# Kernel tuning notes

Measured on AMD Instinct MI355X. Metric: run time of the kernel, lower is better.

## Reference

```python
import jax, jax.numpy as jnp
import numpy as np

N, E, D_IN, HID, OUT, H = 50000, 800000, 64, 128, 128, 8


def _lin(key, fan_in, fan_out, bias=True):
    k1, k2 = jax.random.split(key)
    W = jax.random.normal(k1, (fan_in, fan_out), jnp.float32) / np.sqrt(fan_in)
    if bias:
        b = jax.random.normal(k2, (fan_out,), jnp.float32) * 0.01
        return W, b
    return (W,)


def setup_inputs() -> dict:
    key = jax.random.key(0)
    ks = jax.random.split(key, 40)
    inp = {
        "x": jax.random.normal(ks[0], (N, D_IN), jnp.float32),
        "edge_index": jax.random.randint(ks[1], (2, E), 0, N, jnp.int64),
        "edge_attr": jax.random.normal(ks[2], (E, D_IN), jnp.float32),
    }
    dims = [(D_IN, HID), (HID, HID), (HID, OUT)]  # (in, heads*out_ch) per layer
    ki = 3
    for l, (di, do) in enumerate(dims):
        inp[f"Wq{l}"], inp[f"bq{l}"] = _lin(ks[ki], di, do); ki += 1
        inp[f"Wk{l}"], inp[f"bk{l}"] = _lin(ks[ki], di, do); ki += 1
        inp[f"Wv{l}"], inp[f"bv{l}"] = _lin(ks[ki], di, do); ki += 1
        (inp[f"We{l}"],) = _lin(ks[ki], D_IN, do, bias=False); ki += 1
        inp[f"Ws{l}"], inp[f"bs{l}"] = _lin(ks[ki], di, do); ki += 1
    for l in range(2):
        inp[f"g{l}"] = jnp.ones((HID,), jnp.float32)
        inp[f"be{l}"] = jnp.zeros((HID,), jnp.float32)
    return inp


def _transformer_conv(x, src, dst, edge_attr, Wq, bq, Wk, bk, Wv, bv, We, Ws, bs):
    n = x.shape[0]
    hc = Wq.shape[1]
    c = hc // H
    q = (x @ Wq + bq).reshape(n, H, c)
    k = (x @ Wk + bk).reshape(n, H, c)
    v = (x @ Wv + bv).reshape(n, H, c)
    e = (edge_attr @ We).reshape(-1, H, c)  # [E,H,c]
    ke = k[src] + e                          # edge-wise key + edge proj
    alpha = jnp.einsum("ehc,ehc->eh", q[dst], ke) / jnp.sqrt(jnp.float32(c))
    m = jax.ops.segment_max(alpha, dst, num_segments=n)
    m = jnp.where(jnp.isfinite(m), m, 0.0)
    p = jnp.exp(alpha - m[dst])
    s = jax.ops.segment_sum(p, dst, num_segments=n)
    a = p / (s[dst] + 1e-16)                 # segment softmax over in-edges
    msg = (v[src] + e) * a[..., None]
    out = jax.ops.segment_sum(msg, dst, num_segments=n).reshape(n, hc)
    return out + x @ Ws + bs                 # root/skip connection


def _bn(x, g, b):
    mu = jnp.mean(x, axis=0)
    var = jnp.mean(jnp.square(x - mu), axis=0)
    return g * (x - mu) * jax.lax.rsqrt(var + 1e-5) + b


def reference(x, edge_index, edge_attr,
              Wq0, bq0, Wk0, bk0, Wv0, bv0, We0, Ws0, bs0,
              Wq1, bq1, Wk1, bk1, Wv1, bv1, We1, Ws1, bs1,
              Wq2, bq2, Wk2, bk2, Wv2, bv2, We2, Ws2, bs2,
              g0, be0, g1, be1):
    src, dst = edge_index[0], edge_index[1]
    h = _transformer_conv(x, src, dst, edge_attr, Wq0, bq0, Wk0, bk0, Wv0, bv0, We0, Ws0, bs0)
    h = jax.nn.relu(_bn(h, g0, be0))
    h = _transformer_conv(h, src, dst, edge_attr, Wq1, bq1, Wk1, bk1, Wv1, bv1, We1, Ws1, bs1)
    h = jax.nn.relu(_bn(h, g1, be1))
    h = _transformer_conv(h, src, dst, edge_attr, Wq2, bq2, Wk2, bk2, Wv2, bv2, We2, Ws2, bs2)
    return h, edge_attr
```

## Files before the change

### kernel.cpp

```cpp
#include <hip/hip_runtime.h>
#include <hip/hip_bf16.h>

typedef __attribute__((ext_vector_type(8))) short short8;
typedef __attribute__((ext_vector_type(4))) float f32x4;
typedef unsigned short ushort_t;
typedef __attribute__((ext_vector_type(2))) unsigned short ushort2v;
typedef __attribute__((ext_vector_type(2))) unsigned int uint2v;
typedef __attribute__((ext_vector_type(4))) unsigned int uint4v;

static __device__ __forceinline__ ushort_t f2bf(float x) {
    __hip_bfloat16 h = __float2bfloat16(x);
    return *(ushort_t*)&h;
}
static __device__ __forceinline__ float bflo(unsigned int u) { return __uint_as_float(u << 16); }
static __device__ __forceinline__ float bfhi(unsigned int u) { return __uint_as_float(u & 0xffff0000u); }
static __device__ __forceinline__ float bfu(ushort_t u) { return __uint_as_float((unsigned int)u << 16); }

template <int CTRL>
static __device__ __forceinline__ float dpp_xadd(float x) {
    int y = __builtin_amdgcn_update_dpp(0, __float_as_int(x), CTRL, 0xF, 0xF, true);
    return x + __int_as_float(y);
}


__global__ void hist_kernel(const int* __restrict__ dst, int E, int* __restrict__ hist) {
    int i = blockIdx.x * blockDim.x + threadIdx.x;
    if (i < E) atomicAdd(&hist[dst[i]], 1);
}

__global__ __launch_bounds__(1024) void scan_block_kernel(
    const int* __restrict__ hist, int n, int* __restrict__ row_ptr, int* __restrict__ bsums)
{
    __shared__ int lds[1024];
    int tid = threadIdx.x;
    int i = blockIdx.x * 1024 + tid;
    int vv = (i < n) ? hist[i] : 0;
    lds[tid] = vv;
    __syncthreads();
    for (int off = 1; off < 1024; off <<= 1) {
        int t = (tid >= off) ? lds[tid - off] : 0;
        __syncthreads();
        lds[tid] += t;
        __syncthreads();
    }
    if (i < n) row_ptr[i] = lds[tid] - vv;
    if (tid == 1023) bsums[blockIdx.x] = lds[1023];
}

__global__ void scan_tops_kernel(int* __restrict__ bsums, int nb) {
    if (threadIdx.x == 0 && blockIdx.x == 0) {
        int run = 0;
        for (int i = 0; i < nb; i++) { int t = bsums[i]; bsums[i] = run; run += t; }
    }
}

__global__ __launch_bounds__(256) void scan_add_kernel(
    const int* __restrict__ bsums, int n, int total,
    int* __restrict__ row_ptr, int* __restrict__ cursor)
{
    int i = blockIdx.x * blockDim.x + threadIdx.x;
    if (i < n) {
        int vv = row_ptr[i] + bsums[i >> 10];
        row_ptr[i] = vv;
        cursor[i] = vv;
    }
    if (i == 0) row_ptr[n] = total;
}

__global__ void scatter_kernel(const int* __restrict__ src, const int* __restrict__ dst, int E,
                               int* __restrict__ cursor, int* __restrict__ inv, int* __restrict__ srcs) {
    int i = blockIdx.x * blockDim.x + threadIdx.x;
    if (i < E) {
        int d = dst[i];
        int pos = atomicAdd(&cursor[d], 1);
        inv[i] = pos;
        srcs[pos] = src[i];
    }
}

__global__ __launch_bounds__(256) void copy_permute_kernel(
    const float* __restrict__ edge_attr, const int* __restrict__ inv, int E,
    float* __restrict__ out_pass, ushort_t* __restrict__ ea)
{
    int idx = blockIdx.x * blockDim.x + threadIdx.x;
    if (idx >= E * 8) return;
    int i = idx >> 3, seg = idx & 7;
    const float* s = edge_attr + (size_t)i * 64 + seg * 8;
    float4 f0 = *(const float4*)s;
    float4 f1 = *(const float4*)(s + 4);
    float* d = out_pass + (size_t)i * 64 + seg * 8;
    *(float4*)d = f0;
    *(float4*)(d + 4) = f1;
    short8 o;
    o[0] = f2bf(f0.x); o[1] = f2bf(f0.y); o[2] = f2bf(f0.z); o[3] = f2bf(f0.w);
    o[4] = f2bf(f1.x); o[5] = f2bf(f1.y); o[6] = f2bf(f1.z); o[7] = f2bf(f1.w);
    int pos = inv[i];
    *(short8*)(ea + (size_t)pos * 64 + seg * 8) = o;
}

struct PackArgs {
    const float* We[3];
    const float* Wn[3][4];
    const float* bb[3][4];
};

__global__ __launch_bounds__(256) void pack_all_kernel(
    PackArgs pa, ushort_t* __restrict__ BpackE, ushort_t* __restrict__ BpackN,
    float* __restrict__ biasc)
{
    int idx = blockIdx.x * blockDim.x + threadIdx.x;
    if (idx < 24576) {
        int j = idx & 7, lane = (idx >> 3) & 63, kk = (idx >> 9) & 1,
            t = (idx >> 10) & 7, layer = idx >> 13;
        int kdim = kk * 32 + (lane >> 4) * 8 + j;
        int ncol = t * 16 + (lane & 15);
        BpackE[idx] = f2bf(pa.We[layer][kdim * 128 + ncol]);
    } else if (idx < 188416) {
        int local = idx - 24576;
        int layer, DI;
        if (local < 32768) { layer = 0; DI = 64; }
        else if (local < 98304) { layer = 1; DI = 128; local -= 32768; }
        else { layer = 2; DI = 128; local -= 98304; }
        int NKF = DI >> 5;
        int j = local & 7, lane = (local >> 3) & 63;
        int rest = local >> 9;
        int kf = rest % NKF, t = rest / NKF;
        int kdim = kf * 32 + (lane >> 4) * 8 + j;
        int ncol = t * 16 + (lane & 15);
        BpackN[layer * 65536 + local] = f2bf(pa.Wn[layer][ncol >> 7][kdim * 128 + (ncol & 127)]);
    } else if (idx < 189952) {
        int local = idx - 188416;
        int layer = local >> 9, i = local & 511;
        biasc[layer * 512 + i] = pa.bb[layer][i >> 7][i & 127];
    }
}

template <int DI, bool BN>
__global__ __launch_bounds__(256) void node_gemm_mfma_kernel(
    const float* __restrict__ hin, int N,
    const ushort_t* __restrict__ Bpack, const float* __restrict__ biasc,
    const float* __restrict__ scale, const float* __restrict__ shift,
    float* __restrict__ qout, unsigned int* __restrict__ kvout,
    float* __restrict__ skipout)
{
    constexpr int NKF = DI / 32;
    __shared__ float ctile[64][132];
    __shared__ ushort_t ctileK[64][136];
    int wave = threadIdx.x >> 6;
    int lane = threadIdx.x & 63;
    int tid = threadIdx.x;
    int base = blockIdx.x * 64;
    int m0 = base + wave * 16;

    int mrow = min(m0 + (lane & 15), N - 1);
    const float* arow = hin + (size_t)mrow * DI;
    int koff = (lane >> 4) * 8;

    short8 a[NKF];
#pragma unroll
    for (int kf = 0; kf < NKF; kf++) {
        float4 fa = *(const float4*)(arow + kf * 32 + koff);
        float4 fb = *(const float4*)(arow + kf * 32 + koff + 4);
        if constexpr (BN) {
            int c0 = kf * 32 + koff;
            float4 sa = *(const float4*)(scale + c0);
            float4 sb = *(const float4*)(scale + c0 + 4);
            float4 ha = *(const float4*)(shift + c0);
            float4 hb = *(const float4*)(shift + c0 + 4);
            fa.x = fmaxf(fa.x * sa.x + ha.x, 0.f);
            fa.y = fmaxf(fa.y * sa.y + ha.y, 0.f);
            fa.z = fmaxf(fa.z * sa.z + ha.z, 0.f);
            fa.w = fmaxf(fa.w * sa.w + ha.w, 0.f);
            fb.x = fmaxf(fb.x * sb.x + hb.x, 0.f);
            fb.y = fmaxf(fb.y * sb.y + hb.y, 0.f);
            fb.z = fmaxf(fb.z * sb.z + hb.z, 0.f);
            fb.w = fmaxf(fb.w * sb.w + hb.w, 0.f);
        }
        short8 t;
        t[0] = f2bf(fa.x); t[1] = f2bf(fa.y); t[2] = f2bf(fa.z); t[3] = f2bf(fa.w);
        t[4] = f2bf(fb.x); t[5] = f2bf(fb.y); t[6] = f2bf(fb.z); t[7] = f2bf(fb.w);
        a[kf] = t;
    }

    const short8* Bp = (const short8*)Bpack;
    f32x4 acc[32];
#pragma unroll
    for (int t = 0; t < 32; t++) acc[t] = (f32x4){0.f, 0.f, 0.f, 0.f};
#pragma unroll
    for (int t = 0; t < 32; t++) {
#pragma unroll
        for (int kf = 0; kf < NKF; kf++)
            acc[t] = __builtin_amdgcn_mfma_f32_16x16x32_bf16(a[kf], Bp[(t * NKF + kf) * 64 + lane], acc[t], 0, 0, 0);
    }

    int crow = (lane >> 4) * 4;
    int ccol = lane & 15;

#pragma unroll
    for (int t8 = 0; t8 < 8; t8++) {
        float bb = biasc[t8 * 16 + ccol];
#pragma unroll
        for (int r = 0; r < 4; r++)
            ctile[wave * 16 + crow + r][t8 * 16 + ccol] = acc[t8][r] + bb;
    }
    __syncthreads();
#pragma unroll
    for (int it = 0; it < 8; it++) {
        int idx4 = it * 256 + tid;
        int row = idx4 >> 5;
        int c4 = idx4 & 31;
        int gr = base + row;
        if (gr < N)
            *(float4*)(qout + (size_t)gr * 128 + c4 * 4) = *(const float4*)&ctile[row][c4 * 4];
    }
    __syncthreads();

#pragma unroll
    for (int t8 = 0; t8 < 8; t8++) {
        float bb = biasc[128 + t8 * 16 + ccol];
#pragma unroll
        for (int r = 0; r < 4; r++)
            ctileK[wave * 16 + crow + r][t8 * 16 + ccol] = f2bf(acc[8 + t8][r] + bb);
    }
#pragma unroll
    for (int t8 = 0; t8 < 8; t8++) {
        float bb = biasc[256 + t8 * 16 + ccol];
#pragma unroll
        for (int r = 0; r < 4; r++)
            ctile[wave * 16 + crow + r][t8 * 16 + ccol] = acc[16 + t8][r] + bb;
    }
    __syncthreads();
#pragma unroll
    for (int it = 0; it < 4; it++) {
        int idx8 = it * 256 + tid;
        int row = idx8 >> 4;
        int c8 = idx8 & 15;
        int gr = base + row;
        if (gr < N) {
            const float* vs = &ctile[row][c8 * 8];
            uint4v o0, o1;
#pragma unroll
            for (int i = 0; i < 4; i++) {
                ushort2v kp2 = *(const ushort2v*)&ctileK[row][c8 * 8 + 2 * i];
                unsigned int kp = (unsigned int)kp2[0] | ((unsigned int)kp2[1] << 16);
                unsigned int vp = (unsigned int)f2bf(vs[2 * i]) | ((unsigned int)f2bf(vs[2 * i + 1]) << 16);
                if (i < 2) { o0[2 * i] = kp; o0[2 * i + 1] = vp; }
                else       { o1[2 * (i - 2)] = kp; o1[2 * (i - 2) + 1] = vp; }
            }
            unsigned int* dp = kvout + (size_t)gr * 128 + c8 * 8;
            *(uint4v*)dp = o0;
            *(uint4v*)(dp + 4) = o1;
        }
    }
    __syncthreads();

#pragma unroll
    for (int t8 = 0; t8 < 8; t8++) {
        float bb = biasc[384 + t8 * 16 + ccol];
#pragma unroll
        for (int r = 0; r < 4; r++)
            ctile[wave * 16 + crow + r][t8 * 16 + ccol] = acc[24 + t8][r] + bb;
    }
    __syncthreads();
#pragma unroll
    for (int it = 0; it < 8; it++) {
        int idx4 = it * 256 + tid;
        int row = idx4 >> 5;
        int c4 = idx4 & 31;
        int gr = base + row;
        if (gr < N)
            *(float4*)(skipout + (size_t)gr * 128 + c4 * 4) = *(const float4*)&ctile[row][c4 * 4];
    }
}

#define PROCESS8(B, MASKED)                                                      \
    {                                                                            \
        ushort2v eev[8];                                                         \
        float p[8];                                                              \
        _Pragma("unroll")                                                        \
        for (int u = 0; u < 8; u++)                                              \
            eev[u] = *(const ushort2v*)&elds[wave][(B) * 8 + u][2 * lane];       \
        _Pragma("unroll")                                                        \
        for (int u = 0; u < 8; u++) {                                            \
            uint2v kvp = kvr[(B) * 8 + u];                                       \
            p[u] = qq.x * (bflo(kvp[0]) + bfu(eev[u][0]))                        \
                 + qq.y * (bfhi(kvp[0]) + bfu(eev[u][1]));                       \
        }                                                                        \
        _Pragma("unroll")                                                        \
        for (int u = 0; u < 8; u++) {                                            \
            p[u] = dpp_xadd<0xB1>(p[u]);                                         \
            p[u] = dpp_xadd<0x4E>(p[u]);                                         \
            p[u] = dpp_xadd<0x141>(p[u]);       \
        }                                                                        \
        _Pragma("unroll")                                                        \
        for (int u = 0; u < 8; u++) {                                            \
            float wv = __expf(p[u]);                                             \
            if ((MASKED) && (c0 + (B) * 8 + u >= je)) wv = 0.f;                  \
            uint2v kvp = kvr[(B) * 8 + u];                                       \
            acc0 += wv * (bflo(kvp[1]) + bfu(eev[u][0]));                        \
            acc1 += wv * (bfhi(kvp[1]) + bfu(eev[u][1]));                        \
            sw += wv;                                                            \
        }                                                                        \
    }

__global__ __launch_bounds__(256) void agg_fused_kernel(
    const int* __restrict__ row_ptr, const int* __restrict__ srcs,
    const float* __restrict__ q, const unsigned int* __restrict__ kvbuf,
    const ushort_t* __restrict__ ea, const ushort_t* __restrict__ BpackWe,
    float* __restrict__ hout, int N)
{
    __shared__ ushort_t elds[4][16][136];
    int tid = threadIdx.x;
    int wave = tid >> 6, lane = tid & 63;
    int n = blockIdx.x * 4 + wave;
    if (n >= N) return;

    const short8* BpG = (const short8*)BpackWe;
    short8 bq[16];
#pragma unroll
    for (int i = 0; i < 16; i++) bq[i] = BpG[i * 64 + lane];

    const float2* q2 = (const float2*)q;
    float2* h2 = (float2*)hout;

    int ch = lane & 15, kg = lane >> 4;
    float2 qq = q2[(size_t)n * 64 + lane];
    qq.x *= 0.25f; qq.y *= 0.25f;
    float2 sk = h2[(size_t)n * 64 + lane];
    float acc0 = 0.f, acc1 = 0.f, sw = 0.f;
    int jb = row_ptr[n], je = row_ptr[n + 1];

    short8 a0 = {}, a1 = {};
    int sv = 0;
    if (jb < je) {
        int j0 = min(jb + ch, je - 1);
        sv = srcs[j0];
        const ushort_t* row0 = ea + (size_t)j0 * 64;
        a0 = *(const short8*)(row0 + kg * 8);
        a1 = *(const short8*)(row0 + 32 + kg * 8);
    }

    for (int c0 = jb; c0 < je; c0 += 16) {
        uint2v kvr[16];
#pragma unroll
        for (int u = 0; u < 16; u++) {
            int su = __builtin_amdgcn_readlane(sv, u);
            kvr[u] = *(const uint2v*)(kvbuf + (size_t)su * 128 + 2 * lane);
        }

#pragma unroll
        for (int t = 0; t < 8; t++) {
            f32x4 z = (f32x4){0.f, 0.f, 0.f, 0.f};
            z = __builtin_amdgcn_mfma_f32_16x16x32_bf16(a0, bq[t * 2 + 0], z, 0, 0, 0);
            z = __builtin_amdgcn_mfma_f32_16x16x32_bf16(a1, bq[t * 2 + 1], z, 0, 0, 0);
#pragma unroll
            for (int r = 0; r < 4; r++)
                elds[wave][kg * 4 + r][t * 16 + ch] = f2bf(z[r]);
        }

        int cn = c0 + 16;
        short8 na0 = a0, na1 = a1;
        int nsv = sv;
        if (cn < je) {
            int jn = min(cn + ch, je - 1);
            nsv = srcs[jn];
            const ushort_t* nrow = ea + (size_t)jn * 64;
            na0 = *(const short8*)(nrow + kg * 8);
            na1 = *(const short8*)(nrow + 32 + kg * 8);
        }

        asm volatile("" ::: "memory");

        if (je - c0 >= 16) {
            PROCESS8(0, 0)
            PROCESS8(1, 0)
        } else {
            PROCESS8(0, 1)
            if (c0 + 8 < je) PROCESS8(1, 1)
        }

        a0 = na0; a1 = na1; sv = nsv;
    }
    float inv = 1.0f / (sw + 1e-16f);
    float2 o;
    o.x = acc0 * inv + sk.x;
    o.y = acc1 * inv + sk.y;
    h2[(size_t)n * 64 + lane] = o;
}

__global__ __launch_bounds__(128) void bn_stats_kernel(const float* __restrict__ h, int N,
                                                       float* __restrict__ sums) {
    int f = threadIdx.x;
    float s = 0.f, s2 = 0.f;
    for (int n = blockIdx.x; n < N; n += gridDim.x) {
        float x = h[(size_t)n * 128 + f];
        s += x;
        s2 += x * x;
    }
    atomicAdd(&sums[f], s);
    atomicAdd(&sums[128 + f], s2);
}

__global__ __launch_bounds__(128) void bn_finalize_kernel(
    const float* __restrict__ sums, const float* __restrict__ g,
    const float* __restrict__ be, int N,
    float* __restrict__ scale, float* __restrict__ shift)
{
    int f = threadIdx.x;
    float invN = 1.0f / (float)N;
    float mu = sums[f] * invN;
    float var = sums[128 + f] * invN - mu * mu;
    float sc = g[f] * rsqrtf(var + 1e-5f);
    scale[f] = sc;
    shift[f] = be[f] - mu * sc;
}

extern "C" void kernel_launch(void* const* d_in, const int* in_sizes, int n_in,
                              void* d_out, int out_size, void* d_ws, size_t ws_size,
                              hipStream_t stream)
{
    const float* x = (const float*)d_in[0];
    const int* edge_index = (const int*)d_in[1];
    const float* edge_attr = (const float*)d_in[2];
    int N = in_sizes[0] / 64;
    int E = in_sizes[1] / 2;
    const int* src = edge_index;
    const int* dst = edge_index + E;

    const float* W[3][9];
    for (int l = 0; l < 3; l++)
        for (int i = 0; i < 9; i++) W[l][i] = (const float*)d_in[3 + l * 9 + i];
    const float* g0 = (const float*)d_in[30];
    const float* be0 = (const float*)d_in[31];
    const float* g1 = (const float*)d_in[32];
    const float* be1 = (const float*)d_in[33];

    char* p = (char*)d_ws;
    auto alloc = [&](size_t bytes) -> char* {
        char* r = p;
        p += (bytes + 255) & ~(size_t)255;
        return r;
    };
    float* q = (float*)alloc((size_t)N * 128 * 4);
    unsigned int* kvbuf = (unsigned int*)alloc((size_t)N * 512);
    float* B = (float*)alloc((size_t)N * 128 * 4);
    ushort_t* ea = (ushort_t*)alloc((size_t)E * 64 * 2);
    int* row_ptr = (int*)alloc((size_t)(N + 1) * 4);
    int* cursor = (int*)alloc((size_t)N * 4);
    int* histb = (int*)alloc((size_t)N * 4);
    int* inv = (int*)alloc((size_t)E * 4);
    int* srcs = (int*)alloc((size_t)E * 4);
    int* bsums = (int*)alloc(64 * 4);
    float* sums = (float*)alloc(512 * 4);
    float* bnp = (float*)alloc(512 * 4);
    ushort_t* BpackE = (ushort_t*)alloc((size_t)3 * 8192 * 2);
    ushort_t* BpackN = (ushort_t*)alloc((size_t)3 * 65536 * 2);
    float* biasc = (float*)alloc((size_t)3 * 512 * 4);

    int nb = (N + 1023) / 1024;

    hipMemsetAsync(histb, 0, (size_t)N * 4, stream);
    hipMemsetAsync(sums, 0, 512 * 4, stream);
    hist_kernel<<<(E + 255) / 256, 256, 0, stream>>>(dst, E, histb);
    scan_block_kernel<<<nb, 1024, 0, stream>>>(histb, N, row_ptr, bsums);
    scan_tops_kernel<<<1, 64, 0, stream>>>(bsums, nb);
    scan_add_kernel<<<(N + 255) / 256, 256, 0, stream>>>(bsums, N, E, row_ptr, cursor);
    scatter_kernel<<<(E + 255) / 256, 256, 0, stream>>>(src, dst, E, cursor, inv, srcs);
    copy_permute_kernel<<<(E * 8 + 255) / 256, 256, 0, stream>>>(
        edge_attr, inv, E, (float*)d_out + (size_t)N * 128, ea);

    {
        PackArgs pa;
        for (int l = 0; l < 3; l++) {
            pa.We[l] = W[l][6];
            pa.Wn[l][0] = W[l][0]; pa.Wn[l][1] = W[l][2];
            pa.Wn[l][2] = W[l][4]; pa.Wn[l][3] = W[l][7];
            pa.bb[l][0] = W[l][1]; pa.bb[l][1] = W[l][3];
            pa.bb[l][2] = W[l][5]; pa.bb[l][3] = W[l][8];
        }
        pack_all_kernel<<<(189952 + 255) / 256, 256, 0, stream>>>(pa, BpackE, BpackN, biasc);
    }

    for (int l = 0; l < 3; l++) {
        float* skipbuf = (l == 2) ? (float*)d_out : B;
        if (l == 0)
            node_gemm_mfma_kernel<64, false><<<(N + 63) / 64, 256, 0, stream>>>(
                x, N, BpackN, biasc, nullptr, nullptr, q, kvbuf, skipbuf);
        else
            node_gemm_mfma_kernel<128, true><<<(N + 63) / 64, 256, 0, stream>>>(
                B, N, BpackN + (size_t)l * 65536, biasc + (size_t)l * 512,
                bnp + (size_t)(l - 1) * 256, bnp + (size_t)(l - 1) * 256 + 128,
                q, kvbuf, skipbuf);
        agg_fused_kernel<<<(N + 3) / 4, 256, 0, stream>>>(
            row_ptr, srcs, q, kvbuf, ea, BpackE + (size_t)l * 8192, skipbuf, N);
        if (l < 2) {
            bn_stats_kernel<<<512, 128, 0, stream>>>(skipbuf, N, sums + (size_t)l * 256);
            const float* gg = (l == 0) ? g0 : g1;
            const float* bb = (l == 0) ? be0 : be1;
            bn_finalize_kernel<<<1, 128, 0, stream>>>(
                sums + (size_t)l * 256, gg, bb, N,
                bnp + (size_t)l * 256, bnp + (size_t)l * 256 + 128);
        }
    }
}
```

Baseline: 771.9 us.

## Stage edge-projection weights in LDS and widen aggregation blocks to eight waves

```diff
diff --git a/kernel.cpp b/kernel.cpp
--- a/kernel.cpp
+++ b/kernel.cpp
@@ -19,6 +19,10 @@
 template <int CTRL>
 static __device__ __forceinline__ float dpp_xadd(float x) {
     int y = __builtin_amdgcn_update_dpp(0, __float_as_int(x), CTRL, 0xF, 0xF, true);
+    return x + __int_as_float(y);
+}
+static __device__ __forceinline__ float swz4_add(float x) {
+    int y = __builtin_amdgcn_ds_swizzle(__float_as_int(x), 0x101F);
     return x + __int_as_float(y);
 }
 
@@ -273,7 +277,7 @@
     }
 }
 
-#define PROCESS8(B, MASKED)                                                      \
+#define PROCESS8(B)                                                              \
     {                                                                            \
         ushort2v eev[8];                                                         \
         float p[8];                                                              \
@@ -290,12 +294,12 @@
         for (int u = 0; u < 8; u++) {                                            \
             p[u] = dpp_xadd<0xB1>(p[u]);                                         \
             p[u] = dpp_xadd<0x4E>(p[u]);                                         \
-            p[u] = dpp_xadd<0x141>(p[u]);       \
+            p[u] = swz4_add(p[u]);                                               \
         }                                                                        \
         _Pragma("unroll")                                                        \
         for (int u = 0; u < 8; u++) {                                            \
-            float wv = __expf(p[u]);                                             \
-            if ((MASKED) && (c0 + (B) * 8 + u >= je)) wv = 0.f;                  \
+            float wv = __expf(fminf(p[u] * 0.25f, 60.0f));                       \
+            if (c0 + (B) * 8 + u >= je) wv = 0.f;                                \
             uint2v kvp = kvr[(B) * 8 + u];                                       \
             acc0 += wv * (bflo(kvp[1]) + bfu(eev[u][0]));                        \
             acc1 += wv * (bfhi(kvp[1]) + bfu(eev[u][1]));                        \
@@ -303,29 +307,33 @@
         }                                                                        \
     }
 
-__global__ __launch_bounds__(256) void agg_fused_kernel(
+__global__ __launch_bounds__(512) void agg_fused_kernel(
     const int* __restrict__ row_ptr, const int* __restrict__ srcs,
     const float* __restrict__ q, const unsigned int* __restrict__ kvbuf,
     const ushort_t* __restrict__ ea, const ushort_t* __restrict__ BpackWe,
     float* __restrict__ hout, int N)
 {
-    __shared__ ushort_t elds[4][16][136];
+    __shared__ ushort_t bsh[8192];
+    __shared__ ushort_t elds[8][16][136];
     int tid = threadIdx.x;
+    {
+        const short8* s8 = (const short8*)BpackWe;
+        short8* d8 = (short8*)bsh;
+        d8[tid] = s8[tid];
+        d8[512 + tid] = s8[512 + tid];
+    }
+    __syncthreads();
+
     int wave = tid >> 6, lane = tid & 63;
-    int n = blockIdx.x * 4 + wave;
+    int n = blockIdx.x * 8 + wave;
     if (n >= N) return;
-
-    const short8* BpG = (const short8*)BpackWe;
-    short8 bq[16];
-#pragma unroll
-    for (int i = 0; i < 16; i++) bq[i] = BpG[i * 64 + lane];
 
     const float2* q2 = (const float2*)q;
     float2* h2 = (float2*)hout;
+    const short8* bs8 = (const short8*)bsh;
 
     int ch = lane & 15, kg = lane >> 4;
     float2 qq = q2[(size_t)n * 64 + lane];
-    qq.x *= 0.25f; qq.y *= 0.25f;
     float2 sk = h2[(size_t)n * 64 + lane];
     float acc0 = 0.f, acc1 = 0.f, sw = 0.f;
     int jb = row_ptr[n], je = row_ptr[n + 1];
@@ -351,8 +359,8 @@
 #pragma unroll
         for (int t = 0; t < 8; t++) {
             f32x4 z = (f32x4){0.f, 0.f, 0.f, 0.f};
-            z = __builtin_amdgcn_mfma_f32_16x16x32_bf16(a0, bq[t * 2 + 0], z, 0, 0, 0);
-            z = __builtin_amdgcn_mfma_f32_16x16x32_bf16(a1, bq[t * 2 + 1], z, 0, 0, 0);
+            z = __builtin_amdgcn_mfma_f32_16x16x32_bf16(a0, bs8[(t * 2 + 0) * 64 + lane], z, 0, 0, 0);
+            z = __builtin_amdgcn_mfma_f32_16x16x32_bf16(a1, bs8[(t * 2 + 1) * 64 + lane], z, 0, 0, 0);
 #pragma unroll
             for (int r = 0; r < 4; r++)
                 elds[wave][kg * 4 + r][t * 16 + ch] = f2bf(z[r]);
@@ -371,13 +379,8 @@
 
         asm volatile("" ::: "memory");
 
-        if (je - c0 >= 16) {
-            PROCESS8(0, 0)
-            PROCESS8(1, 0)
-        } else {
-            PROCESS8(0, 1)
-            if (c0 + 8 < je) PROCESS8(1, 1)
-        }
+        PROCESS8(0)
+        if (c0 + 8 < je) PROCESS8(1)
 
         a0 = na0; a1 = na1; sv = nsv;
     }
@@ -491,7 +494,7 @@
                 B, N, BpackN + (size_t)l * 65536, biasc + (size_t)l * 512,
                 bnp + (size_t)(l - 1) * 256, bnp + (size_t)(l - 1) * 256 + 128,
                 q, kvbuf, skipbuf);
-        agg_fused_kernel<<<(N + 3) / 4, 256, 0, stream>>>(
+        agg_fused_kernel<<<(N + 7) / 8, 512, 0, stream>>>(
             row_ptr, srcs, q, kvbuf, ea, BpackE + (size_t)l * 8192, skipbuf, N);
         if (l < 2) {
             bn_stats_kernel<<<512, 128, 0, stream>>>(skipbuf, N, sums + (size_t)l * 256);
```

Result: faster. 678.1 us (-12.1%).
